# Performance work log

Hardware: AMD Instinct MI355X
Metric: run time of the kernel (lower is better)

Reference implementation:

```python
import jax, jax.numpy as jnp
import numpy as np

D_MODEL = 2048
HIDDEN = int(2 * D_MODEL * 4 / 3)  # 5461


def ternary_quant(w):
    # BitNet b1.58-style per-tensor ternary quantization with STE.
    s = jnp.mean(jnp.abs(w))
    q = jnp.clip(jnp.round(w / s), -1.0, 1.0) * s
    return w + jax.lax.stop_gradient(q - w)


def setup_inputs() -> dict:
    key = jax.random.key(0)
    k0, k1, k2, k3 = jax.random.split(key, 4)
    x = jax.random.normal(k0, (4, 4096, D_MODEL), dtype=jnp.float32)
    # torch nn.Linear weights are [out_features, in_features]
    std_in = 1.0 / np.sqrt(D_MODEL)
    std_h = 1.0 / np.sqrt(HIDDEN)
    w1 = jax.random.uniform(k1, (HIDDEN, D_MODEL), jnp.float32, -std_in, std_in)
    w3 = jax.random.uniform(k2, (HIDDEN, D_MODEL), jnp.float32, -std_in, std_in)
    w2 = jax.random.uniform(k3, (D_MODEL, HIDDEN), jnp.float32, -std_h, std_h)
    return {"x": x, "w1": w1, "w3": w3, "w2": w2}


def reference(x, w1, w3, w2):
    w1q = ternary_quant(w1)
    w3q = ternary_quant(w3)
    w2q = ternary_quant(w2)
    h1 = jnp.einsum("bsd,hd->bsh", x, w1q)  # [B,S,H]
    h3 = jnp.einsum("bsd,hd->bsh", x, w3q)  # [B,S,H]
    g = jax.nn.silu(h1) * h3
    return jnp.einsum("bsh,dh->bsd", g, w2q)  # [B,S,D]
```

## Files before the change

### kernel.cpp

```cpp
#include <hip/hip_runtime.h>
#include <cmath>

typedef unsigned short u16;
typedef unsigned char u8;
typedef unsigned int u32;
typedef float f32x4 __attribute__((ext_vector_type(4)));
typedef int i32x4 __attribute__((ext_vector_type(4)));
typedef short s16x8 __attribute__((ext_vector_type(8)));
typedef u32 u32x4 __attribute__((ext_vector_type(4)));

#define D_MODEL 2048
#define HIDDEN  5461
#define HPAD    5504
#define WCNT    11184128
#define XSCALE  4096.0f

__device__ __forceinline__ void async16(const void* g, void* l) {
  __builtin_amdgcn_global_load_lds(
      (const __attribute__((address_space(1))) unsigned int*)g,
      (__attribute__((address_space(3))) unsigned int*)l, 16, 0, 0);
}

__global__ void zero_sums_kernel(double* __restrict__ s) {
  if (threadIdx.x < 3) s[threadIdx.x] = 0.0;
}

__global__ void abssum_kernel(const float* __restrict__ w, long n, double* __restrict__ out) {
  long i0 = ((long)blockIdx.x * blockDim.x + threadIdx.x) * 4;
  long stride = (long)gridDim.x * blockDim.x * 4;
  double s = 0.0;
  for (long i = i0; i < n; i += stride) {
    float4 v = *(const float4*)(w + i);
    s += (double)fabsf(v.x) + (double)fabsf(v.y) + (double)fabsf(v.z) + (double)fabsf(v.w);
  }
#pragma unroll
  for (int off = 32; off > 0; off >>= 1) s += __shfl_down(s, off, 64);
  __shared__ double ls[4];
  int lane = threadIdx.x & 63, wv = threadIdx.x >> 6;
  if (lane == 0) ls[wv] = s;
  __syncthreads();
  if (threadIdx.x == 0) atomicAdd(out, ls[0] + ls[1] + ls[2] + ls[3]);
}

__global__ void quant13_kernel(const float* __restrict__ w, const double* __restrict__ sum,
                               char* __restrict__ ws) {
  double s = *sum * (1.0 / (double)WCNT);
  int nt = blockIdx.x;
  int c  = blockIdx.y * 256 + threadIdx.x;
  int col = c & 127;
  int kg  = c >> 7;
  int n = nt * 128 + col;
  u32x4 qv = {0u, 0u, 0u, 0u};
  if (n < HIDDEN) {
    const float* row = w + (long)n * D_MODEL + kg * 16;
#pragma unroll
    for (int q4 = 0; q4 < 4; ++q4) {
      float4 v = *(const float4*)(row + q4 * 4);
      float vv[4] = {v.x, v.y, v.z, v.w};
      u32 word = 0;
#pragma unroll
      for (int e = 0; e < 4; ++e) {
        int qi = (int)fmin(fmax(rint((double)vv[e] / s), -1.0), 1.0);
        word |= ((u32)(u8)(char)qi) << (8 * e);
      }
      qv[q4] = word;
    }
  }
  *(u32x4*)(ws + (long)nt * 262144 + ((long)kg * 128 + col) * 16) = qv;
}

__global__ void quant2_kernel(const float* __restrict__ w, const double* __restrict__ sum,
                              char* __restrict__ ws) {
  double s = *sum * (1.0 / (double)WCNT);
  int nt = blockIdx.x;
  int kg = blockIdx.y;
  int col = threadIdx.x;
  int n = nt * 256 + col;
  const float* row = w + (long)n * HIDDEN;
  u32x4 qv = {0u, 0u, 0u, 0u};
#pragma unroll
  for (int q4 = 0; q4 < 4; ++q4) {
    u32 word = 0;
#pragma unroll
    for (int e = 0; e < 4; ++e) {
      int k = kg * 16 + q4 * 4 + e;
      int qi = 0;
      if (k < HIDDEN) {
        float v = row[k];
        qi = (int)fmin(fmax(rint((double)v / s), -1.0), 1.0);
      }
      word |= ((u32)(u8)(char)qi) << (8 * e);
    }
    qv[q4] = word;
  }
  *(u32x4*)(ws + (long)nt * 1409024 + ((long)kg * 256 + col) * 16) = qv;
}

__global__ void xquant_kernel(const float* __restrict__ x, u8* __restrict__ xhi,
                              u8* __restrict__ xlo) {
  int mt = blockIdx.x;
  int c  = blockIdx.y * 256 + threadIdx.x;
  int row = c & 127;
  int kg  = c >> 7;
  const float* src = x + ((long)mt * 128 + row) * D_MODEL + kg * 16;
  u32x4 hv, lv;
#pragma unroll
  for (int q4 = 0; q4 < 4; ++q4) {
    float4 v = *(const float4*)(src + q4 * 4);
    float vv[4] = {v.x, v.y, v.z, v.w};
    u32 hw = 0, lw = 0;
#pragma unroll
    for (int e = 0; e < 4; ++e) {
      float f = fminf(fmaxf(vv[e] * XSCALE, -32639.f), 32639.f);
      int tt = (int)rintf(f) + 128;
      hw |= ((u32)((tt >> 8) & 0xFF)) << (8 * e);
      lw |= ((u32)((tt ^ 0x80) & 0xFF)) << (8 * e);
    }
    hv[q4] = hw; lv[q4] = lw;
  }
  long o = (long)mt * 262144 + ((long)kg * 128 + row) * 16;
  *(u32x4*)(xhi + o) = hv;
  *(u32x4*)(xlo + o) = lv;
}

__global__ __launch_bounds__(256, 1)
void gemm1_kernel(const u8* __restrict__ xhi, const u8* __restrict__ xlo,
                  const char* __restrict__ w1s, const char* __restrict__ w3s,
                  const double* __restrict__ sums, u8* __restrict__ gshi,
                  u8* __restrict__ gslo, int mt0) {
  __shared__ alignas(16) u8 L[3 * 32768];
  const int mtl = blockIdx.x;
  const int ntt = blockIdx.y;
  const int t = threadIdx.x;
  const int lane = t & 63, wave = t >> 6;
  const int wm = wave >> 1, wn = wave & 1;
  const int quad = lane >> 4;
  const int rowA = wm * 64 + (lane & 15);
  const int colB = wn * 64 + (lane & 15);

  i32x4 a1h[4][4], a1l[4][4], a3h[4][4], a3l[4][4];
#pragma unroll
  for (int i = 0; i < 4; ++i)
#pragma unroll
    for (int j = 0; j < 4; ++j) {
      a1h[i][j] = {0, 0, 0, 0}; a1l[i][j] = {0, 0, 0, 0};
      a3h[i][j] = {0, 0, 0, 0}; a3l[i][j] = {0, 0, 0, 0};
    }

  const u8* Ah = xhi + (long)(mt0 + mtl) * 262144 + t * 16;
  const u8* Al = xlo + (long)(mt0 + mtl) * 262144 + t * 16;
  const char* B1 = w1s + (long)ntt * 262144 + t * 16;
  const char* B3 = w3s + (long)ntt * 262144 + t * 16;

#define STAGE1(buf, c) do {                                      \
    u8* Lb_ = L + (buf) * 32768;                                 \
    async16(Ah + (c) * 8192,        Lb_ + t * 16);               \
    async16(Ah + (c) * 8192 + 4096, Lb_ + 4096 + t * 16);        \
    async16(Al + (c) * 8192,        Lb_ + 8192 + t * 16);        \
    async16(Al + (c) * 8192 + 4096, Lb_ + 12288 + t * 16);       \
    async16(B1 + (c) * 8192,        Lb_ + 16384 + t * 16);       \
    async16(B1 + (c) * 8192 + 4096, Lb_ + 20480 + t * 16);       \
    async16(B3 + (c) * 8192,        Lb_ + 24576 + t * 16);       \
    async16(B3 + (c) * 8192 + 4096, Lb_ + 28672 + t * 16);       \
  } while (0)

  STAGE1(0, 0);
  int cur = 0;
  for (int c = 0; c < 32; ++c) {
    int nb = cur + 1; if (nb == 3) nb = 0;
    if (c < 31) {
      STAGE1(nb, c + 1);
      asm volatile("s_waitcnt vmcnt(8)" ::: "memory");
    } else {
      asm volatile("s_waitcnt vmcnt(0)" ::: "memory");
    }
    __builtin_amdgcn_s_barrier();
    const u8* Lb = L + cur * 32768;
    i32x4 ah[4], al[4], b1f[4], b3f[4];
#pragma unroll
    for (int j = 0; j < 4; ++j) {
      b1f[j] = *(const i32x4*)&Lb[16384 + (quad * 128 + colB + j * 16) * 16];
      b3f[j] = *(const i32x4*)&Lb[24576 + (quad * 128 + colB + j * 16) * 16];
    }
#pragma unroll
    for (int i = 0; i < 4; ++i) {
      ah[i] = *(const i32x4*)&Lb[(quad * 128 + rowA + i * 16) * 16];
      al[i] = *(const i32x4*)&Lb[8192 + (quad * 128 + rowA + i * 16) * 16];
    }
    __builtin_amdgcn_s_setprio(1);
#pragma unroll
    for (int i = 0; i < 4; ++i)
#pragma unroll
      for (int j = 0; j < 4; ++j) {
        a1h[i][j] = __builtin_amdgcn_mfma_i32_16x16x64_i8(ah[i], b1f[j], a1h[i][j], 0, 0, 0);
        a1l[i][j] = __builtin_amdgcn_mfma_i32_16x16x64_i8(al[i], b1f[j], a1l[i][j], 0, 0, 0);
        a3h[i][j] = __builtin_amdgcn_mfma_i32_16x16x64_i8(ah[i], b3f[j], a3h[i][j], 0, 0, 0);
        a3l[i][j] = __builtin_amdgcn_mfma_i32_16x16x64_i8(al[i], b3f[j], a3l[i][j], 0, 0, 0);
      }
    __builtin_amdgcn_s_setprio(0);
    cur = nb;
  }
#undef STAGE1

  const float sc1 = (float)(sums[0] * (1.0 / (double)WCNT)) / XSCALE;
  const float sc3 = (float)(sums[1] * (1.0 / (double)WCNT)) / XSCALE;
  u8* gh = gshi + (long)mtl * 704512;
  u8* gl = gslo + (long)mtl * 704512;
#pragma unroll
  for (int i = 0; i < 4; ++i) {
#pragma unroll
    for (int j = 0; j < 4; ++j) {
      const int h = ntt * 128 + wn * 64 + j * 16 + (lane & 15);
      const long cbase = ((long)(h >> 4) * 128) * 16 + (h & 15);
#pragma unroll
      for (int rr = 0; rr < 4; ++rr) {
        const int mm = wm * 64 + i * 16 + quad * 4 + rr;
        float h1 = (float)(a1h[i][j][rr] * 256 + a1l[i][j][rr]) * sc1;
        float h3 = (float)(a3h[i][j][rr] * 256 + a3l[i][j][rr]) * sc3;
        float g = (h1 / (1.0f + expf(-h1))) * h3;
        float f = fminf(fmaxf(g * XSCALE, -32639.f), 32639.f);
        int tt2 = (int)rintf(f) + 128;
        long off = cbase + (long)mm * 16;
        gh[off] = (u8)((tt2 >> 8) & 0xFF);
        gl[off] = (u8)((tt2 ^ 0x80) & 0xFF);
      }
    }
  }
}

__global__ __launch_bounds__(256, 1)
void gemm2_kernel(const u8* __restrict__ gshi, const u8* __restrict__ gslo,
                  const char* __restrict__ w2s, const double* __restrict__ sums,
                  float* __restrict__ out) {
  __shared__ alignas(16) u8 L[3 * 32768];
  const int mtl = blockIdx.x;
  const int ntt = blockIdx.y;
  const int t = threadIdx.x;
  const int lane = t & 63, wave = t >> 6;
  const int wm = wave >> 1, wn = wave & 1;
  const int quad = lane >> 4;
  const int rowA = wm * 64 + (lane & 15);
  const int colB = wn * 128 + (lane & 15);

  i32x4 ach[4][8], acl[4][8];
#pragma unroll
  for (int i = 0; i < 4; ++i)
#pragma unroll
    for (int j = 0; j < 8; ++j) {
      ach[i][j] = {0, 0, 0, 0}; acl[i][j] = {0, 0, 0, 0};
    }

  const u8* Ahg = gshi + (long)mtl * 704512 + t * 16;
  const u8* Alg = gslo + (long)mtl * 704512 + t * 16;
  const char* Bw = w2s + (long)ntt * 1409024 + t * 16;

#define STAGE2(buf, c) do {                                      \
    u8* Lb_ = L + (buf) * 32768;                                 \
    async16(Ahg + (c) * 8192,         Lb_ + t * 16);             \
    async16(Ahg + (c) * 8192 + 4096,  Lb_ + 4096 + t * 16);      \
    async16(Alg + (c) * 8192,         Lb_ + 8192 + t * 16);      \
    async16(Alg + (c) * 8192 + 4096,  Lb_ + 12288 + t * 16);     \
    async16(Bw + (c) * 16384,         Lb_ + 16384 + t * 16);     \
    async16(Bw + (c) * 16384 + 4096,  Lb_ + 20480 + t * 16);     \
    async16(Bw + (c) * 16384 + 8192,  Lb_ + 24576 + t * 16);     \
    async16(Bw + (c) * 16384 + 12288, Lb_ + 28672 + t * 16);     \
  } while (0)

  STAGE2(0, 0);
  int cur = 0;
  for (int c = 0; c < 86; ++c) {
    int nb = cur + 1; if (nb == 3) nb = 0;
    if (c < 85) {
      STAGE2(nb, c + 1);
      asm volatile("s_waitcnt vmcnt(8)" ::: "memory");
    } else {
      asm volatile("s_waitcnt vmcnt(0)" ::: "memory");
    }
    __builtin_amdgcn_s_barrier();
    const u8* Lb = L + cur * 32768;
    i32x4 ah[4], al[4], bw[8];
#pragma unroll
    for (int j = 0; j < 8; ++j)
      bw[j] = *(const i32x4*)&Lb[16384 + (quad * 256 + colB + j * 16) * 16];
#pragma unroll
    for (int i = 0; i < 4; ++i) {
      ah[i] = *(const i32x4*)&Lb[(quad * 128 + rowA + i * 16) * 16];
      al[i] = *(const i32x4*)&Lb[8192 + (quad * 128 + rowA + i * 16) * 16];
    }
    __builtin_amdgcn_s_setprio(1);
#pragma unroll
    for (int i = 0; i < 4; ++i)
#pragma unroll
      for (int j = 0; j < 8; ++j) {
        ach[i][j] = __builtin_amdgcn_mfma_i32_16x16x64_i8(ah[i], bw[j], ach[i][j], 0, 0, 0);
        acl[i][j] = __builtin_amdgcn_mfma_i32_16x16x64_i8(al[i], bw[j], acl[i][j], 0, 0, 0);
      }
    __builtin_amdgcn_s_setprio(0);
    cur = nb;
  }
#undef STAGE2

  const float s2g = (float)(sums[2] * (1.0 / (double)WCNT)) / XSCALE;
#pragma unroll
  for (int i = 0; i < 4; ++i) {
#pragma unroll
    for (int j = 0; j < 8; ++j) {
      const int d = ntt * 256 + wn * 128 + j * 16 + (lane & 15);
#pragma unroll
      for (int rr = 0; rr < 4; ++rr) {
        const long m = (long)mtl * 128 + wm * 64 + i * 16 + quad * 4 + rr;
        int v = ach[i][j][rr] * 256 + acl[i][j][rr];
        out[m * D_MODEL + d] = (float)v * s2g;
      }
    }
  }
}

extern "C" void kernel_launch(void* const* d_in, const int* in_sizes, int n_in,
                              void* d_out, int out_size, void* d_ws, size_t ws_size,
                              hipStream_t stream) {
  (void)in_sizes; (void)n_in; (void)out_size; (void)ws_size;
  const float* x  = (const float*)d_in[0];
  const float* w1 = (const float*)d_in[1];
  const float* w3 = (const float*)d_in[2];
  const float* w2 = (const float*)d_in[3];
  float* out = (float*)d_out;

  char* ws = (char*)d_ws;
  double* sums = (double*)ws;
  char* w1s = ws + 256;
  char* w3s = w1s + 11272192L;
  char* w2s = w3s + 11272192L;
  u8*   xhi = (u8*)(w2s + 11272192L);
  u8*   xlo = xhi + 33554432L;
  u8*   gshi = xlo + 33554432L;
  u8*   gslo = gshi + 45088768L;

  zero_sums_kernel<<<1, 64, 0, stream>>>(sums);
  abssum_kernel<<<1024, 256, 0, stream>>>(w1, (long)WCNT, sums + 0);
  abssum_kernel<<<1024, 256, 0, stream>>>(w3, (long)WCNT, sums + 1);
  abssum_kernel<<<1024, 256, 0, stream>>>(w2, (long)WCNT, sums + 2);

  quant13_kernel<<<dim3(43, 64), 256, 0, stream>>>(w1, sums + 0, w1s);
  quant13_kernel<<<dim3(43, 64), 256, 0, stream>>>(w3, sums + 1, w3s);
  quant2_kernel<<<dim3(8, 344), 256, 0, stream>>>(w2, sums + 2, w2s);
  xquant_kernel<<<dim3(128, 64), 256, 0, stream>>>(x, xhi, xlo);

  for (int pass = 0; pass < 2; ++pass) {
    gemm1_kernel<<<dim3(64, 43), 256, 0, stream>>>(xhi, xlo, w1s, w3s, sums,
                                                   gshi, gslo, pass * 64);
    gemm2_kernel<<<dim3(64, 8), 256, 0, stream>>>(gshi, gslo, w2s, sums,
                                                  out + (long)pass * 64 * 128 * D_MODEL);
  }
}
```

Measured before the change: 1.521 ms.

## Shrink GEMM N-tiles to 64 and run two blocks per CU

Narrows the weight tile width from 128 (gemm1) and 256 (gemm2) to 64 columns. The packed weight layouts and quantization kernels are reworked to match, and launch bounds are raised to allow two workgroups per CU. Fewer accumulators and less LDS per block are meant to raise occupancy and improve grid fill and latency hiding. gemm2 also swaps its grid order so N-tiles vary fastest. The cost is lower arithmetic intensity per block: A tiles are reloaded more often and global/L2 traffic increases.

Measured after the change: 1.334 ms. 1.14x faster.

```diff
diff --git a/kernel.cpp b/kernel.cpp
--- a/kernel.cpp
+++ b/kernel.cpp
@@ -47,9 +47,9 @@
   double s = *sum * (1.0 / (double)WCNT);
   int nt = blockIdx.x;
   int c  = blockIdx.y * 256 + threadIdx.x;
-  int col = c & 127;
-  int kg  = c >> 7;
-  int n = nt * 128 + col;
+  int col = c & 63;
+  int kg  = c >> 6;
+  int n = nt * 64 + col;
   u32x4 qv = {0u, 0u, 0u, 0u};
   if (n < HIDDEN) {
     const float* row = w + (long)n * D_MODEL + kg * 16;
@@ -66,7 +66,7 @@
       qv[q4] = word;
     }
   }
-  *(u32x4*)(ws + (long)nt * 262144 + ((long)kg * 128 + col) * 16) = qv;
+  *(u32x4*)(ws + (long)nt * 131072 + ((long)kg * 64 + col) * 16) = qv;
 }
 
 __global__ void quant2_kernel(const float* __restrict__ w, const double* __restrict__ sum,
@@ -74,26 +74,22 @@
   double s = *sum * (1.0 / (double)WCNT);
   int nt = blockIdx.x;
   int kg = blockIdx.y;
-  int col = threadIdx.x;
-  int n = nt * 256 + col;
+  int col = threadIdx.x & 63;
+  int q4  = threadIdx.x >> 6;
+  int n = nt * 64 + col;
   const float* row = w + (long)n * HIDDEN;
-  u32x4 qv = {0u, 0u, 0u, 0u};
-#pragma unroll
-  for (int q4 = 0; q4 < 4; ++q4) {
-    u32 word = 0;
-#pragma unroll
-    for (int e = 0; e < 4; ++e) {
-      int k = kg * 16 + q4 * 4 + e;
-      int qi = 0;
-      if (k < HIDDEN) {
-        float v = row[k];
-        qi = (int)fmin(fmax(rint((double)v / s), -1.0), 1.0);
-      }
-      word |= ((u32)(u8)(char)qi) << (8 * e);
-    }
-    qv[q4] = word;
-  }
-  *(u32x4*)(ws + (long)nt * 1409024 + ((long)kg * 256 + col) * 16) = qv;
+  u32 word = 0;
+#pragma unroll
+  for (int e = 0; e < 4; ++e) {
+    int k = kg * 16 + q4 * 4 + e;
+    int qi = 0;
+    if (k < HIDDEN) {
+      float v = row[k];
+      qi = (int)fmin(fmax(rint((double)v / s), -1.0), 1.0);
+    }
+    word |= ((u32)(u8)(char)qi) << (8 * e);
+  }
+  *(u32*)(ws + (long)nt * 352256 + ((long)kg * 64 + col) * 16 + q4 * 4) = word;
 }
 
 __global__ void xquant_kernel(const float* __restrict__ x, u8* __restrict__ xhi,
@@ -123,45 +119,44 @@
   *(u32x4*)(xlo + o) = lv;
 }
 
-__global__ __launch_bounds__(256, 1)
+__global__ __launch_bounds__(256, 2)
 void gemm1_kernel(const u8* __restrict__ xhi, const u8* __restrict__ xlo,
                   const char* __restrict__ w1s, const char* __restrict__ w3s,
                   const double* __restrict__ sums, u8* __restrict__ gshi,
                   u8* __restrict__ gslo, int mt0) {
-  __shared__ alignas(16) u8 L[3 * 32768];
+  __shared__ alignas(16) u8 L[3 * 24576];
   const int mtl = blockIdx.x;
-  const int ntt = blockIdx.y;
+  const int nt  = blockIdx.y;
+  const int mtg = mt0 + mtl;
   const int t = threadIdx.x;
   const int lane = t & 63, wave = t >> 6;
   const int wm = wave >> 1, wn = wave & 1;
   const int quad = lane >> 4;
   const int rowA = wm * 64 + (lane & 15);
-  const int colB = wn * 64 + (lane & 15);
-
-  i32x4 a1h[4][4], a1l[4][4], a3h[4][4], a3l[4][4];
+  const int rowB = wn * 32 + (lane & 15);
+
+  i32x4 a1h[4][2], a1l[4][2], a3h[4][2], a3l[4][2];
 #pragma unroll
   for (int i = 0; i < 4; ++i)
 #pragma unroll
-    for (int j = 0; j < 4; ++j) {
+    for (int j = 0; j < 2; ++j) {
       a1h[i][j] = {0, 0, 0, 0}; a1l[i][j] = {0, 0, 0, 0};
       a3h[i][j] = {0, 0, 0, 0}; a3l[i][j] = {0, 0, 0, 0};
     }
 
-  const u8* Ah = xhi + (long)(mt0 + mtl) * 262144 + t * 16;
-  const u8* Al = xlo + (long)(mt0 + mtl) * 262144 + t * 16;
-  const char* B1 = w1s + (long)ntt * 262144 + t * 16;
-  const char* B3 = w3s + (long)ntt * 262144 + t * 16;
+  const u8* Ah = xhi + (long)mtg * 262144 + t * 16;
+  const u8* Al = xlo + (long)mtg * 262144 + t * 16;
+  const char* B1 = w1s + (long)nt * 131072 + t * 16;
+  const char* B3 = w3s + (long)nt * 131072 + t * 16;
 
 #define STAGE1(buf, c) do {                                      \
-    u8* Lb_ = L + (buf) * 32768;                                 \
+    u8* Lb_ = L + (buf) * 24576;                                 \
     async16(Ah + (c) * 8192,        Lb_ + t * 16);               \
     async16(Ah + (c) * 8192 + 4096, Lb_ + 4096 + t * 16);        \
     async16(Al + (c) * 8192,        Lb_ + 8192 + t * 16);        \
     async16(Al + (c) * 8192 + 4096, Lb_ + 12288 + t * 16);       \
-    async16(B1 + (c) * 8192,        Lb_ + 16384 + t * 16);       \
-    async16(B1 + (c) * 8192 + 4096, Lb_ + 20480 + t * 16);       \
-    async16(B3 + (c) * 8192,        Lb_ + 24576 + t * 16);       \
-    async16(B3 + (c) * 8192 + 4096, Lb_ + 28672 + t * 16);       \
+    async16(B1 + (c) * 4096,        Lb_ + 16384 + t * 16);       \
+    async16(B3 + (c) * 4096,        Lb_ + 20480 + t * 16);       \
   } while (0)
 
   STAGE1(0, 0);
@@ -170,28 +165,28 @@
     int nb = cur + 1; if (nb == 3) nb = 0;
     if (c < 31) {
       STAGE1(nb, c + 1);
-      asm volatile("s_waitcnt vmcnt(8)" ::: "memory");
+      asm volatile("s_waitcnt vmcnt(6)" ::: "memory");
     } else {
       asm volatile("s_waitcnt vmcnt(0)" ::: "memory");
     }
     __builtin_amdgcn_s_barrier();
-    const u8* Lb = L + cur * 32768;
-    i32x4 ah[4], al[4], b1f[4], b3f[4];
-#pragma unroll
-    for (int j = 0; j < 4; ++j) {
-      b1f[j] = *(const i32x4*)&Lb[16384 + (quad * 128 + colB + j * 16) * 16];
-      b3f[j] = *(const i32x4*)&Lb[24576 + (quad * 128 + colB + j * 16) * 16];
+    const u8* Lb = L + cur * 24576;
+    i32x4 b1f[2], b3f[2], ah[4], al[4];
+#pragma unroll
+    for (int j = 0; j < 2; ++j) {
+      b1f[j] = *(const i32x4*)&Lb[16384 + quad * 1024 + (rowB + j * 16) * 16];
+      b3f[j] = *(const i32x4*)&Lb[20480 + quad * 1024 + (rowB + j * 16) * 16];
     }
 #pragma unroll
     for (int i = 0; i < 4; ++i) {
-      ah[i] = *(const i32x4*)&Lb[(quad * 128 + rowA + i * 16) * 16];
-      al[i] = *(const i32x4*)&Lb[8192 + (quad * 128 + rowA + i * 16) * 16];
+      ah[i] = *(const i32x4*)&Lb[quad * 2048 + (rowA + i * 16) * 16];
+      al[i] = *(const i32x4*)&Lb[8192 + quad * 2048 + (rowA + i * 16) * 16];
     }
     __builtin_amdgcn_s_setprio(1);
 #pragma unroll
     for (int i = 0; i < 4; ++i)
 #pragma unroll
-      for (int j = 0; j < 4; ++j) {
+      for (int j = 0; j < 2; ++j) {
         a1h[i][j] = __builtin_amdgcn_mfma_i32_16x16x64_i8(ah[i], b1f[j], a1h[i][j], 0, 0, 0);
         a1l[i][j] = __builtin_amdgcn_mfma_i32_16x16x64_i8(al[i], b1f[j], a1l[i][j], 0, 0, 0);
         a3h[i][j] = __builtin_amdgcn_mfma_i32_16x16x64_i8(ah[i], b3f[j], a3h[i][j], 0, 0, 0);
@@ -209,8 +204,8 @@
 #pragma unroll
   for (int i = 0; i < 4; ++i) {
 #pragma unroll
-    for (int j = 0; j < 4; ++j) {
-      const int h = ntt * 128 + wn * 64 + j * 16 + (lane & 15);
+    for (int j = 0; j < 2; ++j) {
+      const int h = nt * 64 + wn * 32 + j * 16 + (lane & 15);
       const long cbase = ((long)(h >> 4) * 128) * 16 + (h & 15);
 #pragma unroll
       for (int rr = 0; rr < 4; ++rr) {
@@ -228,42 +223,39 @@
   }
 }
 
-__global__ __launch_bounds__(256, 1)
+__global__ __launch_bounds__(256, 2)
 void gemm2_kernel(const u8* __restrict__ gshi, const u8* __restrict__ gslo,
                   const char* __restrict__ w2s, const double* __restrict__ sums,
                   float* __restrict__ out) {
-  __shared__ alignas(16) u8 L[3 * 32768];
-  const int mtl = blockIdx.x;
-  const int ntt = blockIdx.y;
+  __shared__ alignas(16) u8 L[3 * 20480];
+  const int ntt = blockIdx.x;
+  const int mtl = blockIdx.y;
   const int t = threadIdx.x;
   const int lane = t & 63, wave = t >> 6;
   const int wm = wave >> 1, wn = wave & 1;
   const int quad = lane >> 4;
   const int rowA = wm * 64 + (lane & 15);
-  const int colB = wn * 128 + (lane & 15);
-
-  i32x4 ach[4][8], acl[4][8];
+  const int colB = wn * 32 + (lane & 15);
+
+  i32x4 ach[4][2], acl[4][2];
 #pragma unroll
   for (int i = 0; i < 4; ++i)
 #pragma unroll
-    for (int j = 0; j < 8; ++j) {
+    for (int j = 0; j < 2; ++j) {
       ach[i][j] = {0, 0, 0, 0}; acl[i][j] = {0, 0, 0, 0};
     }
 
   const u8* Ahg = gshi + (long)mtl * 704512 + t * 16;
   const u8* Alg = gslo + (long)mtl * 704512 + t * 16;
-  const char* Bw = w2s + (long)ntt * 1409024 + t * 16;
+  const char* Bw = w2s + (long)ntt * 352256 + t * 16;
 
 #define STAGE2(buf, c) do {                                      \
-    u8* Lb_ = L + (buf) * 32768;                                 \
-    async16(Ahg + (c) * 8192,         Lb_ + t * 16);             \
-    async16(Ahg + (c) * 8192 + 4096,  Lb_ + 4096 + t * 16);      \
-    async16(Alg + (c) * 8192,         Lb_ + 8192 + t * 16);      \
-    async16(Alg + (c) * 8192 + 4096,  Lb_ + 12288 + t * 16);     \
-    async16(Bw + (c) * 16384,         Lb_ + 16384 + t * 16);     \
-    async16(Bw + (c) * 16384 + 4096,  Lb_ + 20480 + t * 16);     \
-    async16(Bw + (c) * 16384 + 8192,  Lb_ + 24576 + t * 16);     \
-    async16(Bw + (c) * 16384 + 12288, Lb_ + 28672 + t * 16);     \
+    u8* Lb_ = L + (buf) * 20480;                                 \
+    async16(Ahg + (c) * 8192,        Lb_ + t * 16);              \
+    async16(Ahg + (c) * 8192 + 4096, Lb_ + 4096 + t * 16);       \
+    async16(Alg + (c) * 8192,        Lb_ + 8192 + t * 16);       \
+    async16(Alg + (c) * 8192 + 4096, Lb_ + 12288 + t * 16);     \
+    async16(Bw + (c) * 4096,         Lb_ + 16384 + t * 16);      \
   } while (0)
 
   STAGE2(0, 0);
@@ -272,26 +264,26 @@
     int nb = cur + 1; if (nb == 3) nb = 0;
     if (c < 85) {
       STAGE2(nb, c + 1);
-      asm volatile("s_waitcnt vmcnt(8)" ::: "memory");
+      asm volatile("s_waitcnt vmcnt(5)" ::: "memory");
     } else {
       asm volatile("s_waitcnt vmcnt(0)" ::: "memory");
     }
     __builtin_amdgcn_s_barrier();
-    const u8* Lb = L + cur * 32768;
-    i32x4 ah[4], al[4], bw[8];
-#pragma unroll
-    for (int j = 0; j < 8; ++j)
-      bw[j] = *(const i32x4*)&Lb[16384 + (quad * 256 + colB + j * 16) * 16];
+    const u8* Lb = L + cur * 20480;
+    i32x4 ah[4], al[4], bw[2];
+#pragma unroll
+    for (int j = 0; j < 2; ++j)
+      bw[j] = *(const i32x4*)&Lb[16384 + quad * 1024 + (colB + j * 16) * 16];
 #pragma unroll
     for (int i = 0; i < 4; ++i) {
-      ah[i] = *(const i32x4*)&Lb[(quad * 128 + rowA + i * 16) * 16];
-      al[i] = *(const i32x4*)&Lb[8192 + (quad * 128 + rowA + i * 16) * 16];
+      ah[i] = *(const i32x4*)&Lb[quad * 2048 + (rowA + i * 16) * 16];
+      al[i] = *(const i32x4*)&Lb[8192 + quad * 2048 + (rowA + i * 16) * 16];
     }
     __builtin_amdgcn_s_setprio(1);
 #pragma unroll
     for (int i = 0; i < 4; ++i)
 #pragma unroll
-      for (int j = 0; j < 8; ++j) {
+      for (int j = 0; j < 2; ++j) {
         ach[i][j] = __builtin_amdgcn_mfma_i32_16x16x64_i8(ah[i], bw[j], ach[i][j], 0, 0, 0);
         acl[i][j] = __builtin_amdgcn_mfma_i32_16x16x64_i8(al[i], bw[j], acl[i][j], 0, 0, 0);
       }
@@ -304,8 +296,8 @@
 #pragma unroll
   for (int i = 0; i < 4; ++i) {
 #pragma unroll
-    for (int j = 0; j < 8; ++j) {
-      const int d = ntt * 256 + wn * 128 + j * 16 + (lane & 15);
+    for (int j = 0; j < 2; ++j) {
+      const int d = ntt * 64 + wn * 32 + j * 16 + (lane & 15);
 #pragma unroll
       for (int rr = 0; rr < 4; ++rr) {
         const long m = (long)mtl * 128 + wm * 64 + i * 16 + quad * 4 + rr;
@@ -341,15 +333,15 @@
   abssum_kernel<<<1024, 256, 0, stream>>>(w3, (long)WCNT, sums + 1);
   abssum_kernel<<<1024, 256, 0, stream>>>(w2, (long)WCNT, sums + 2);
 
-  quant13_kernel<<<dim3(43, 64), 256, 0, stream>>>(w1, sums + 0, w1s);
-  quant13_kernel<<<dim3(43, 64), 256, 0, stream>>>(w3, sums + 1, w3s);
-  quant2_kernel<<<dim3(8, 344), 256, 0, stream>>>(w2, sums + 2, w2s);
+  quant13_kernel<<<dim3(86, 32), 256, 0, stream>>>(w1, sums + 0, w1s);
+  quant13_kernel<<<dim3(86, 32), 256, 0, stream>>>(w3, sums + 1, w3s);
+  quant2_kernel<<<dim3(32, 344), 256, 0, stream>>>(w2, sums + 2, w2s);
   xquant_kernel<<<dim3(128, 64), 256, 0, stream>>>(x, xhi, xlo);
 
   for (int pass = 0; pass < 2; ++pass) {
-    gemm1_kernel<<<dim3(64, 43), 256, 0, stream>>>(xhi, xlo, w1s, w3s, sums,
+    gemm1_kernel<<<dim3(64, 86), 256, 0, stream>>>(xhi, xlo, w1s, w3s, sums,
                                                    gshi, gslo, pass * 64);
-    gemm2_kernel<<<dim3(64, 8), 256, 0, stream>>>(gshi, gslo, w2s, sums,
-                                                  out + (long)pass * 64 * 128 * D_MODEL);
-  }
-}
+    gemm2_kernel<<<dim3(32, 64), 256, 0, stream>>>(gshi, gslo, w2s, sums,
+                                                   out + (long)pass * 64 * 128 * D_MODEL);
+  }
+}
```
